# Optimization experiments

Hardware: AMD Instinct MI355X
Metric: run time of the kernel (lower is better)

The kernel has to match this reference:

```python
import jax, jax.numpy as jnp
import numpy as np

ALPHA = 0.05
NUM_LAYERS = 2


def setup_inputs() -> dict:
    key = jax.random.key(0)
    k1, k2, k3, k4, k5 = jax.random.split(key, 5)
    N, F, C, E = 100000, 64, 40, 1600000
    x = jax.random.normal(k1, (N, F), dtype=jnp.float32)
    edge_attr = jax.random.uniform(k2, (E,), dtype=jnp.float32)
    lin_w = jax.random.normal(k3, (F, C), dtype=jnp.float32) * (1.0 / np.sqrt(F))
    lin_b = jax.random.normal(k4, (C,), dtype=jnp.float32) * 0.01
    edge_index = jax.random.randint(k5, (2, E), 0, N, dtype=jnp.int64)
    return {"x": x, "edge_attr": edge_attr, "lin_w": lin_w, "lin_b": lin_b,
            "edge_index": edge_index}


def reference(x, edge_attr, lin_w, lin_b, edge_index):
    N = x.shape[0]
    row, col = edge_index[0], edge_index[1]
    # symmetric GCN normalization with edge weights
    deg = jax.ops.segment_sum(edge_attr, col, num_segments=N)  # [N]
    dis = jnp.where(deg > 0, jax.lax.rsqrt(jnp.maximum(deg, 1e-12)), 0.0)
    norm = dis[row] * edge_attr * dis[col]  # [E]

    def conv(h):
        # gather source features, scale, scatter-add to targets
        return jax.ops.segment_sum(norm[:, None] * h[row], col, num_segments=N)

    x_input = ALPHA * x
    scale = (1.0 - ALPHA) / NUM_LAYERS
    h = x
    acc = jnp.zeros_like(x)
    for _ in range(NUM_LAYERS):
        h = conv(h)
        acc = acc + scale * h
    out = acc + x_input
    logits = out @ lin_w + lin_b
    return jax.nn.log_softmax(logits, axis=1)
```

## Files before the change

### kernel.cpp

```cpp
#include <hip/hip_runtime.h>
#include <math.h>
#include <string.h>


#define ALPHA  0.05f
#define SCALE  0.475f
#define FDIM   64
#define CDIM   40
#define NPAD   131072
#define CHUNK  8192
#define BCAP   10240
#define SRCMASK 0x1FFFFu

__device__ __forceinline__ unsigned short f2bf(float f) {
    unsigned u = __float_as_uint(f);
    unsigned r = (u + 0x7FFFu + ((u >> 16) & 1u)) >> 16;
    return (unsigned short)r;
}
__device__ __forceinline__ float bfLo(unsigned u) { return __uint_as_float(u << 16); }
__device__ __forceinline__ float bfHi(unsigned u) { return __uint_as_float(u & 0xffff0000u); }
__device__ __forceinline__ float wUnpack(unsigned v) {
    return __uint_as_float((v >> 17) << 16);
}

__global__ __launch_bounds__(1024) void part_scatter(
        const int* __restrict__ row, const int* __restrict__ col,
        const float* __restrict__ ea, int* __restrict__ alloc,
        int2* __restrict__ ppay, int E) {
    __shared__ unsigned h[256];
    __shared__ unsigned offs[256];
    int tid = threadIdx.x, blk = blockIdx.x;
    if (tid < 256) h[tid] = 0;
    __syncthreads();
    int base = blk * CHUNK;
    int end  = min(base + CHUNK, E);
    for (int e = base + tid; e < end; e += 1024)
        atomicAdd(&h[col[e] >> 9], 1u);
    __syncthreads();
    if (tid < 256) {
        unsigned hc = h[tid];
        unsigned r = hc ? (unsigned)atomicAdd(&alloc[tid], (int)hc) : 0u;
        offs[tid] = (unsigned)(tid * BCAP) + r;
    }
    __syncthreads();
    for (int e = base + tid; e < end; e += 1024) {
        int c = col[e];
        int bin = c >> 9;
        unsigned p = atomicAdd(&offs[bin], 1u);
        if (p < (unsigned)((bin + 1) * BCAP))
            ppay[p] = make_int2(row[e] | ((c & 511) << 20), __float_as_int(ea[e]));
    }
}

__global__ __launch_bounds__(256) void bucket_base(const int* __restrict__ alloc,
                                                   int* __restrict__ bb) {
    __shared__ int s[256];
    int tid = threadIdx.x;
    int v = min(alloc[tid], BCAP);
    s[tid] = v;
    __syncthreads();
    for (int off = 1; off < 256; off <<= 1) {
        int t = (tid >= off) ? s[tid - off] : 0;
        __syncthreads();
        s[tid] += t;
        __syncthreads();
    }
    bb[tid] = s[tid] - v;
    if (tid == 255) bb[256] = s[255];
}

__global__ __launch_bounds__(256) void bucket_csr(
        const int2* __restrict__ ppay, const int* __restrict__ alloc,
        const int* __restrict__ bb, int* __restrict__ start,
        unsigned* __restrict__ csr, float* __restrict__ dis, int N) {
    __shared__ unsigned cnt8[512][8];
    __shared__ unsigned ps[256], exc[512];
    __shared__ float sdeg[512];
    int tid = threadIdx.x, k = blockIdx.x;
    int cnt = min(alloc[k], BCAP);
    int e0  = bb[k];
    const int2* src = ppay + (size_t)k * BCAP;

    for (int i = tid; i < 4096; i += 256) ((unsigned*)cnt8)[i] = 0;
    sdeg[tid] = 0.0f; sdeg[tid + 256] = 0.0f;
    __syncthreads();

    for (int j = tid; j < cnt; j += 256) {
        int2 pay = src[j];
        int c = (pay.x >> 20) & 511;
        atomicAdd(&cnt8[c][(pay.x & 0xFFFFF) >> 14], 1u);
        atomicAdd(&sdeg[c], __int_as_float(pay.y));
    }
    __syncthreads();

    int c0 = 2 * tid, c1 = 2 * tid + 1;
    unsigned t0 = 0, t1 = 0;
    #pragma unroll
    for (int o = 0; o < 8; ++o) { t0 += cnt8[c0][o]; t1 += cnt8[c1][o]; }
    unsigned pair = t0 + t1;
    ps[tid] = pair;
    __syncthreads();
    for (int off = 1; off < 256; off <<= 1) {
        unsigned t = (tid >= off) ? ps[tid - off] : 0;
        __syncthreads();
        ps[tid] += t;
        __syncthreads();
    }
    unsigned pexc = ps[tid] - pair;
    exc[c0] = pexc;
    exc[c1] = pexc + t0;
    unsigned b = pexc;
    #pragma unroll
    for (int o = 0; o < 8; ++o) { unsigned t = cnt8[c0][o]; cnt8[c0][o] = b; b += t; }
    b = pexc + t0;
    #pragma unroll
    for (int o = 0; o < 8; ++o) { unsigned t = cnt8[c1][o]; cnt8[c1][o] = b; b += t; }
    __syncthreads();

    #pragma unroll
    for (int i = tid; i < 512; i += 256) {
        int g = k * 512 + i;
        if (g <= N) start[g] = e0 + (int)exc[i];
        if (g < N) {
            float d = sdeg[i];
            dis[g] = (d > 0.0f) ? rsqrtf(fmaxf(d, 1e-12f)) : 0.0f;
        }
    }

    for (int j = tid; j < cnt; j += 256) {
        int2 pay = src[j];
        int c    = (pay.x >> 20) & 511;
        int srcn = pay.x & 0xFFFFF;
        unsigned p = atomicAdd(&cnt8[c][srcn >> 14], 1u);
        unsigned wbf = (unsigned)f2bf(__int_as_float(pay.y));
        csr[e0 + p] = (unsigned)srcn | (wbf << 17);
    }
}

__global__ void csr_scale_kernel(unsigned* __restrict__ csr,
                                 const float* __restrict__ dis, int E) {
    int stride = gridDim.x * blockDim.x;
    for (int e = blockIdx.x * blockDim.x + threadIdx.x; e < E; e += stride) {
        unsigned v = csr[e];
        unsigned src = v & SRCMASK;
        float w = wUnpack(v) * dis[src];
        csr[e] = src | ((unsigned)f2bf(w) << 17);
    }
}

__global__ __launch_bounds__(256) void lin_kernel(
        const float* __restrict__ x, const float* __restrict__ W,
        unsigned* __restrict__ ybf, int N) {
    __shared__ float sWt[CDIM][FDIM + 4];
    for (int i = threadIdx.x; i < FDIM * CDIM; i += 256) {
        int k = i / CDIM, c = i - k * CDIM;
        sWt[c][k] = W[i];
    }
    __syncthreads();

    int t = threadIdx.x;
    int node = blockIdx.x * 64 + (t >> 2);
    if (node >= N) return;
    int cs = (t & 3) * 10;

    float acc[10];
    #pragma unroll
    for (int i = 0; i < 10; ++i) acc[i] = 0.0f;

    const float4* xr = (const float4*)(x + (size_t)node * FDIM);
    #pragma unroll
    for (int k4 = 0; k4 < FDIM / 4; ++k4) {
        float4 v = xr[k4];
        #pragma unroll
        for (int i = 0; i < 10; ++i) {
            const float4 w = *(const float4*)&sWt[cs + i][k4 * 4];
            acc[i] = fmaf(v.x, w.x, fmaf(v.y, w.y, fmaf(v.z, w.z, fmaf(v.w, w.w, acc[i]))));
        }
    }

    unsigned* yr = ybf + (size_t)node * (CDIM / 2) + (t & 3) * 5;
    #pragma unroll
    for (int k = 0; k < 5; ++k)
        yr[k] = (unsigned)f2bf(acc[2 * k]) | ((unsigned)f2bf(acc[2 * k + 1]) << 16);
}

__global__ __launch_bounds__(256) void spmv_kernel(
        const unsigned* __restrict__ gin, const int* __restrict__ start,
        const unsigned* __restrict__ csr, const float* __restrict__ dis,
        unsigned* __restrict__ gout, int N) {
    int lane = threadIdx.x & 63;
    int wid  = threadIdx.x >> 6;
    int grp  = lane / 20;
    int grel = lane - grp * 20;
    int node = blockIdx.x * 12 + wid * 3 + grp;
    bool act = (grp < 3) && (node < N);

    int e0 = 0, e1 = 0;
    if (act) { e0 = start[node]; e1 = start[node + 1]; }

    float aL0 = 0, aL1 = 0, aL2 = 0, aL3 = 0;
    float aH0 = 0, aH1 = 0, aH2 = 0, aH3 = 0;
    int j = e0;
    for (; j + 7 < e1; j += 8) {
        unsigned v0 = csr[j],     v1 = csr[j + 1], v2 = csr[j + 2], v3 = csr[j + 3];
        unsigned v4 = csr[j + 4], v5 = csr[j + 5], v6 = csr[j + 6], v7 = csr[j + 7];
        unsigned u0 = gin[(size_t)(v0 & SRCMASK) * 20 + grel];
        unsigned u1 = gin[(size_t)(v1 & SRCMASK) * 20 + grel];
        unsigned u2 = gin[(size_t)(v2 & SRCMASK) * 20 + grel];
        unsigned u3 = gin[(size_t)(v3 & SRCMASK) * 20 + grel];
        unsigned u4 = gin[(size_t)(v4 & SRCMASK) * 20 + grel];
        unsigned u5 = gin[(size_t)(v5 & SRCMASK) * 20 + grel];
        unsigned u6 = gin[(size_t)(v6 & SRCMASK) * 20 + grel];
        unsigned u7 = gin[(size_t)(v7 & SRCMASK) * 20 + grel];
        float w0 = wUnpack(v0), w1 = wUnpack(v1), w2 = wUnpack(v2), w3 = wUnpack(v3);
        float w4 = wUnpack(v4), w5 = wUnpack(v5), w6 = wUnpack(v6), w7 = wUnpack(v7);
        aL0 = fmaf(w0, bfLo(u0), aL0); aH0 = fmaf(w0, bfHi(u0), aH0);
        aL1 = fmaf(w1, bfLo(u1), aL1); aH1 = fmaf(w1, bfHi(u1), aH1);
        aL2 = fmaf(w2, bfLo(u2), aL2); aH2 = fmaf(w2, bfHi(u2), aH2);
        aL3 = fmaf(w3, bfLo(u3), aL3); aH3 = fmaf(w3, bfHi(u3), aH3);
        aL0 = fmaf(w4, bfLo(u4), aL0); aH0 = fmaf(w4, bfHi(u4), aH0);
        aL1 = fmaf(w5, bfLo(u5), aL1); aH1 = fmaf(w5, bfHi(u5), aH1);
        aL2 = fmaf(w6, bfLo(u6), aL2); aH2 = fmaf(w6, bfHi(u6), aH2);
        aL3 = fmaf(w7, bfLo(u7), aL3); aH3 = fmaf(w7, bfHi(u7), aH3);
    }
    for (; j < e1; ++j) {
        unsigned v = csr[j];
        unsigned u = gin[(size_t)(v & SRCMASK) * 20 + grel];
        float w = wUnpack(v);
        aL0 = fmaf(w, bfLo(u), aL0); aH0 = fmaf(w, bfHi(u), aH0);
    }
    if (act) {
        float dn = dis[node];
        float lo = dn * ((aL0 + aL1) + (aL2 + aL3));
        float hi = dn * ((aH0 + aH1) + (aH2 + aH3));
        gout[(size_t)node * 20 + grel] = (unsigned)f2bf(lo) | ((unsigned)f2bf(hi) << 16);
    }
}

__global__ __launch_bounds__(256) void spmv_final_kernel(
        const unsigned* __restrict__ g1, const unsigned* __restrict__ y,
        const float* __restrict__ bias, const int* __restrict__ start,
        const unsigned* __restrict__ csr, const float* __restrict__ dis,
        float* __restrict__ out, int N) {
    int lane = threadIdx.x & 63;
    int wid  = threadIdx.x >> 6;
    int grp  = lane / 20;
    int grel = lane - grp * 20;
    int node = blockIdx.x * 12 + wid * 3 + grp;
    bool act = (grp < 3) && (node < N);

    int e0 = 0, e1 = 0;
    if (act) { e0 = start[node]; e1 = start[node + 1]; }

    float aL0 = 0, aL1 = 0, aL2 = 0, aL3 = 0;
    float aH0 = 0, aH1 = 0, aH2 = 0, aH3 = 0;
    int j = e0;
    for (; j + 7 < e1; j += 8) {
        unsigned v0 = csr[j],     v1 = csr[j + 1], v2 = csr[j + 2], v3 = csr[j + 3];
        unsigned v4 = csr[j + 4], v5 = csr[j + 5], v6 = csr[j + 6], v7 = csr[j + 7];
        unsigned u0 = g1[(size_t)(v0 & SRCMASK) * 20 + grel];
        unsigned u1 = g1[(size_t)(v1 & SRCMASK) * 20 + grel];
        unsigned u2 = g1[(size_t)(v2 & SRCMASK) * 20 + grel];
        unsigned u3 = g1[(size_t)(v3 & SRCMASK) * 20 + grel];
        unsigned u4 = g1[(size_t)(v4 & SRCMASK) * 20 + grel];
        unsigned u5 = g1[(size_t)(v5 & SRCMASK) * 20 + grel];
        unsigned u6 = g1[(size_t)(v6 & SRCMASK) * 20 + grel];
        unsigned u7 = g1[(size_t)(v7 & SRCMASK) * 20 + grel];
        float w0 = wUnpack(v0), w1 = wUnpack(v1), w2 = wUnpack(v2), w3 = wUnpack(v3);
        float w4 = wUnpack(v4), w5 = wUnpack(v5), w6 = wUnpack(v6), w7 = wUnpack(v7);
        aL0 = fmaf(w0, bfLo(u0), aL0); aH0 = fmaf(w0, bfHi(u0), aH0);
        aL1 = fmaf(w1, bfLo(u1), aL1); aH1 = fmaf(w1, bfHi(u1), aH1);
        aL2 = fmaf(w2, bfLo(u2), aL2); aH2 = fmaf(w2, bfHi(u2), aH2);
        aL3 = fmaf(w3, bfLo(u3), aL3); aH3 = fmaf(w3, bfHi(u3), aH3);
        aL0 = fmaf(w4, bfLo(u4), aL0); aH0 = fmaf(w4, bfHi(u4), aH0);
        aL1 = fmaf(w5, bfLo(u5), aL1); aH1 = fmaf(w5, bfHi(u5), aH1);
        aL2 = fmaf(w6, bfLo(u6), aL2); aH2 = fmaf(w6, bfHi(u6), aH2);
        aL3 = fmaf(w7, bfLo(u7), aL3); aH3 = fmaf(w7, bfHi(u7), aH3);
    }
    for (; j < e1; ++j) {
        unsigned v = csr[j];
        unsigned u = g1[(size_t)(v & SRCMASK) * 20 + grel];
        float w = wUnpack(v);
        aL0 = fmaf(w, bfLo(u), aL0); aH0 = fmaf(w, bfHi(u), aH0);
    }

    float logitL = 0.0f, logitH = 0.0f;
    if (act) {
        float dn  = dis[node];
        float g2L = dn * ((aL0 + aL1) + (aL2 + aL3));
        float g2H = dn * ((aH0 + aH1) + (aH2 + aH3));
        unsigned yu = y[(size_t)node * 20 + grel];
        unsigned gu = g1[(size_t)node * 20 + grel];
        float2 bv = *(const float2*)&bias[2 * grel];
        logitL = fmaf(ALPHA, bfLo(yu), fmaf(SCALE, bfLo(gu) + g2L, bv.x));
        logitH = fmaf(ALPHA, bfHi(yu), fmaf(SCALE, bfHi(gu) + g2H, bv.y));
    }

    float m = act ? fmaxf(logitL, logitH) : -INFINITY;
    #pragma unroll
    for (int off = 16; off; off >>= 1) {
        float o = __shfl(m, lane + off);
        if (grel + off < 20) m = fmaxf(m, o);
    }
    m = __shfl(m, grp * 20);

    float ex = act ? (expf(logitL - m) + expf(logitH - m)) : 0.0f;
    #pragma unroll
    for (int off = 16; off; off >>= 1) {
        float o = __shfl(ex, lane + off);
        if (grel + off < 20) ex += o;
    }
    ex = __shfl(ex, grp * 20);

    if (act) {
        float lse = m + logf(ex);
        float2 o;
        o.x = logitL - lse;
        o.y = logitH - lse;
        double dv;
        memcpy(&dv, &o, 8);
        __builtin_nontemporal_store(dv, (double*)&out[(size_t)node * CDIM + 2 * grel]);
    }
}

extern "C" void kernel_launch(void* const* d_in, const int* in_sizes, int n_in,
                              void* d_out, int out_size, void* d_ws, size_t ws_size,
                              hipStream_t stream) {
    const float* x  = (const float*)d_in[0];
    const float* ea = (const float*)d_in[1];
    const float* W  = (const float*)d_in[2];
    const float* b  = (const float*)d_in[3];
    const int*   ei = (const int*)d_in[4];

    const int N = in_sizes[0] / FDIM;
    const int E = in_sizes[1];
    const int* row = ei;
    const int* col = ei + E;

    const int NBLK = (E + CHUNK - 1) / CHUNK;

    int*   startp = (int*)d_ws;
    float* dis    = (float*)(startp + NPAD);
    int*   alloc  = (int*)(dis + NPAD);
    int*   bb     = alloc + 1024;
    int2*  ppay   = (int2*)(bb + 1024);
    unsigned* csr = (unsigned*)(ppay + 256 * BCAP);
    unsigned* g1bf = csr + E;
    unsigned* ybf  = (unsigned*)ppay;

    hipMemsetAsync(alloc, 0, 256 * sizeof(int), stream);

    part_scatter<<<NBLK, 1024, 0, stream>>>(row, col, ea, alloc, ppay, E);
    bucket_base <<<1, 256, 0, stream>>>(alloc, bb);
    bucket_csr  <<<256, 256, 0, stream>>>(ppay, alloc, bb, startp, csr, dis, N);
    csr_scale_kernel<<<2048, 256, 0, stream>>>(csr, dis, E);
    lin_kernel  <<<(N + 63) / 64, 256, 0, stream>>>(x, W, ybf, N);

    int spmv_blocks = (N + 11) / 12;
    spmv_kernel      <<<spmv_blocks, 256, 0, stream>>>(ybf, startp, csr, dis, g1bf, N);
    spmv_final_kernel<<<spmv_blocks, 256, 0, stream>>>(g1bf, ybf, b, startp, csr, dis,
                                                       (float*)d_out, N);
}
```

Before: 157.5 us.

## Use merge-path edge-balanced SpMV partitioning and fold bucket prefix scan into CSR build

```diff
diff --git a/kernel.cpp b/kernel.cpp
--- a/kernel.cpp
+++ b/kernel.cpp
@@ -10,6 +10,7 @@
 #define NPAD   131072
 #define CHUNK  8192
 #define BCAP   10240
+#define CE     64
 #define SRCMASK 0x1FFFFu
 
 __device__ __forceinline__ unsigned short f2bf(float f) {
@@ -52,33 +53,28 @@
     }
 }
 
-__global__ __launch_bounds__(256) void bucket_base(const int* __restrict__ alloc,
-                                                   int* __restrict__ bb) {
-    __shared__ int s[256];
-    int tid = threadIdx.x;
-    int v = min(alloc[tid], BCAP);
-    s[tid] = v;
-    __syncthreads();
-    for (int off = 1; off < 256; off <<= 1) {
-        int t = (tid >= off) ? s[tid - off] : 0;
-        __syncthreads();
-        s[tid] += t;
-        __syncthreads();
-    }
-    bb[tid] = s[tid] - v;
-    if (tid == 255) bb[256] = s[255];
-}
-
 __global__ __launch_bounds__(256) void bucket_csr(
         const int2* __restrict__ ppay, const int* __restrict__ alloc,
-        const int* __restrict__ bb, int* __restrict__ start,
-        unsigned* __restrict__ csr, float* __restrict__ dis, int N) {
+        int* __restrict__ start, unsigned* __restrict__ csr,
+        float* __restrict__ dis, int N) {
     __shared__ unsigned cnt8[512][8];
     __shared__ unsigned ps[256], exc[512];
     __shared__ float sdeg[512];
+    __shared__ int sAll[256];
     int tid = threadIdx.x, k = blockIdx.x;
+
+    sAll[tid] = min(alloc[tid], BCAP);
+    __syncthreads();
+    int v = sAll[tid];
+    for (int off = 1; off < 256; off <<= 1) {
+        int t = (tid >= off) ? sAll[tid - off] : 0;
+        __syncthreads();
+        sAll[tid] += t;
+        __syncthreads();
+    }
+    int e0  = sAll[k] - min(alloc[k], BCAP);
     int cnt = min(alloc[k], BCAP);
-    int e0  = bb[k];
+    (void)v;
     const int2* src = ppay + (size_t)k * BCAP;
 
     for (int i = tid; i < 4096; i += 256) ((unsigned*)cnt8)[i] = 0;
@@ -184,142 +180,149 @@
         yr[k] = (unsigned)f2bf(acc[2 * k]) | ((unsigned)f2bf(acc[2 * k + 1]) << 16);
 }
 
-__global__ __launch_bounds__(256) void spmv_kernel(
+__global__ __launch_bounds__(256) void spmv_mp(
         const unsigned* __restrict__ gin, const int* __restrict__ start,
         const unsigned* __restrict__ csr, const float* __restrict__ dis,
-        unsigned* __restrict__ gout, int N) {
+        unsigned* __restrict__ gout, int N, int E, int G) {
     int lane = threadIdx.x & 63;
     int wid  = threadIdx.x >> 6;
     int grp  = lane / 20;
     int grel = lane - grp * 20;
-    int node = blockIdx.x * 12 + wid * 3 + grp;
-    bool act = (grp < 3) && (node < N);
-
-    int e0 = 0, e1 = 0;
-    if (act) { e0 = start[node]; e1 = start[node + 1]; }
-
-    float aL0 = 0, aL1 = 0, aL2 = 0, aL3 = 0;
-    float aH0 = 0, aH1 = 0, aH2 = 0, aH3 = 0;
-    int j = e0;
-    for (; j + 7 < e1; j += 8) {
-        unsigned v0 = csr[j],     v1 = csr[j + 1], v2 = csr[j + 2], v3 = csr[j + 3];
-        unsigned v4 = csr[j + 4], v5 = csr[j + 5], v6 = csr[j + 6], v7 = csr[j + 7];
-        unsigned u0 = gin[(size_t)(v0 & SRCMASK) * 20 + grel];
-        unsigned u1 = gin[(size_t)(v1 & SRCMASK) * 20 + grel];
-        unsigned u2 = gin[(size_t)(v2 & SRCMASK) * 20 + grel];
-        unsigned u3 = gin[(size_t)(v3 & SRCMASK) * 20 + grel];
-        unsigned u4 = gin[(size_t)(v4 & SRCMASK) * 20 + grel];
-        unsigned u5 = gin[(size_t)(v5 & SRCMASK) * 20 + grel];
-        unsigned u6 = gin[(size_t)(v6 & SRCMASK) * 20 + grel];
-        unsigned u7 = gin[(size_t)(v7 & SRCMASK) * 20 + grel];
-        float w0 = wUnpack(v0), w1 = wUnpack(v1), w2 = wUnpack(v2), w3 = wUnpack(v3);
-        float w4 = wUnpack(v4), w5 = wUnpack(v5), w6 = wUnpack(v6), w7 = wUnpack(v7);
-        aL0 = fmaf(w0, bfLo(u0), aL0); aH0 = fmaf(w0, bfHi(u0), aH0);
-        aL1 = fmaf(w1, bfLo(u1), aL1); aH1 = fmaf(w1, bfHi(u1), aH1);
-        aL2 = fmaf(w2, bfLo(u2), aL2); aH2 = fmaf(w2, bfHi(u2), aH2);
-        aL3 = fmaf(w3, bfLo(u3), aL3); aH3 = fmaf(w3, bfHi(u3), aH3);
-        aL0 = fmaf(w4, bfLo(u4), aL0); aH0 = fmaf(w4, bfHi(u4), aH0);
-        aL1 = fmaf(w5, bfLo(u5), aL1); aH1 = fmaf(w5, bfHi(u5), aH1);
-        aL2 = fmaf(w6, bfLo(u6), aL2); aH2 = fmaf(w6, bfHi(u6), aH2);
-        aL3 = fmaf(w7, bfLo(u7), aL3); aH3 = fmaf(w7, bfHi(u7), aH3);
-    }
-    for (; j < e1; ++j) {
-        unsigned v = csr[j];
-        unsigned u = gin[(size_t)(v & SRCMASK) * 20 + grel];
-        float w = wUnpack(v);
-        aL0 = fmaf(w, bfLo(u), aL0); aH0 = fmaf(w, bfHi(u), aH0);
-    }
-    if (act) {
-        float dn = dis[node];
-        float lo = dn * ((aL0 + aL1) + (aL2 + aL3));
-        float hi = dn * ((aH0 + aH1) + (aH2 + aH3));
-        gout[(size_t)node * 20 + grel] = (unsigned)f2bf(lo) | ((unsigned)f2bf(hi) << 16);
-    }
-}
-
-__global__ __launch_bounds__(256) void spmv_final_kernel(
+    int g = blockIdx.x * 12 + wid * 3 + grp;
+    bool act = (grp < 3) && (g < G);
+    int lo  = act ? g * CE : (E + 2);
+    int hiR = min(lo + CE, E + 1);
+
+    int a = 0, b = N;
+    while (a < b) { int mid = (a + b) >> 1; if (start[mid] < lo) a = mid + 1; else b = mid; }
+
+    int n = a;
+    while (n < N && start[n] < hiR) {
+        int e0 = start[n], e1 = start[n + 1];
+        float aL0 = 0, aL1 = 0, aL2 = 0, aL3 = 0;
+        float aH0 = 0, aH1 = 0, aH2 = 0, aH3 = 0;
+        int j = e0;
+        for (; j + 7 < e1; j += 8) {
+            unsigned v0 = csr[j],     v1 = csr[j + 1], v2 = csr[j + 2], v3 = csr[j + 3];
+            unsigned v4 = csr[j + 4], v5 = csr[j + 5], v6 = csr[j + 6], v7 = csr[j + 7];
+            unsigned u0 = gin[(size_t)(v0 & SRCMASK) * 20 + grel];
+            unsigned u1 = gin[(size_t)(v1 & SRCMASK) * 20 + grel];
+            unsigned u2 = gin[(size_t)(v2 & SRCMASK) * 20 + grel];
+            unsigned u3 = gin[(size_t)(v3 & SRCMASK) * 20 + grel];
+            unsigned u4 = gin[(size_t)(v4 & SRCMASK) * 20 + grel];
+            unsigned u5 = gin[(size_t)(v5 & SRCMASK) * 20 + grel];
+            unsigned u6 = gin[(size_t)(v6 & SRCMASK) * 20 + grel];
+            unsigned u7 = gin[(size_t)(v7 & SRCMASK) * 20 + grel];
+            float w0 = wUnpack(v0), w1 = wUnpack(v1), w2 = wUnpack(v2), w3 = wUnpack(v3);
+            float w4 = wUnpack(v4), w5 = wUnpack(v5), w6 = wUnpack(v6), w7 = wUnpack(v7);
+            aL0 = fmaf(w0, bfLo(u0), aL0); aH0 = fmaf(w0, bfHi(u0), aH0);
+            aL1 = fmaf(w1, bfLo(u1), aL1); aH1 = fmaf(w1, bfHi(u1), aH1);
+            aL2 = fmaf(w2, bfLo(u2), aL2); aH2 = fmaf(w2, bfHi(u2), aH2);
+            aL3 = fmaf(w3, bfLo(u3), aL3); aH3 = fmaf(w3, bfHi(u3), aH3);
+            aL0 = fmaf(w4, bfLo(u4), aL0); aH0 = fmaf(w4, bfHi(u4), aH0);
+            aL1 = fmaf(w5, bfLo(u5), aL1); aH1 = fmaf(w5, bfHi(u5), aH1);
+            aL2 = fmaf(w6, bfLo(u6), aL2); aH2 = fmaf(w6, bfHi(u6), aH2);
+            aL3 = fmaf(w7, bfLo(u7), aL3); aH3 = fmaf(w7, bfHi(u7), aH3);
+        }
+        for (; j < e1; ++j) {
+            unsigned v = csr[j];
+            unsigned u = gin[(size_t)(v & SRCMASK) * 20 + grel];
+            float w = wUnpack(v);
+            aL0 = fmaf(w, bfLo(u), aL0); aH0 = fmaf(w, bfHi(u), aH0);
+        }
+        float dn = dis[n];
+        float lov = dn * ((aL0 + aL1) + (aL2 + aL3));
+        float hiv = dn * ((aH0 + aH1) + (aH2 + aH3));
+        gout[(size_t)n * 20 + grel] = (unsigned)f2bf(lov) | ((unsigned)f2bf(hiv) << 16);
+        ++n;
+    }
+}
+
+__global__ __launch_bounds__(256) void spmv_final_mp(
         const unsigned* __restrict__ g1, const unsigned* __restrict__ y,
         const float* __restrict__ bias, const int* __restrict__ start,
         const unsigned* __restrict__ csr, const float* __restrict__ dis,
-        float* __restrict__ out, int N) {
+        float* __restrict__ out, int N, int E, int G) {
     int lane = threadIdx.x & 63;
     int wid  = threadIdx.x >> 6;
     int grp  = lane / 20;
     int grel = lane - grp * 20;
-    int node = blockIdx.x * 12 + wid * 3 + grp;
-    bool act = (grp < 3) && (node < N);
-
-    int e0 = 0, e1 = 0;
-    if (act) { e0 = start[node]; e1 = start[node + 1]; }
-
-    float aL0 = 0, aL1 = 0, aL2 = 0, aL3 = 0;
-    float aH0 = 0, aH1 = 0, aH2 = 0, aH3 = 0;
-    int j = e0;
-    for (; j + 7 < e1; j += 8) {
-        unsigned v0 = csr[j],     v1 = csr[j + 1], v2 = csr[j + 2], v3 = csr[j + 3];
-        unsigned v4 = csr[j + 4], v5 = csr[j + 5], v6 = csr[j + 6], v7 = csr[j + 7];
-        unsigned u0 = g1[(size_t)(v0 & SRCMASK) * 20 + grel];
-        unsigned u1 = g1[(size_t)(v1 & SRCMASK) * 20 + grel];
-        unsigned u2 = g1[(size_t)(v2 & SRCMASK) * 20 + grel];
-        unsigned u3 = g1[(size_t)(v3 & SRCMASK) * 20 + grel];
-        unsigned u4 = g1[(size_t)(v4 & SRCMASK) * 20 + grel];
-        unsigned u5 = g1[(size_t)(v5 & SRCMASK) * 20 + grel];
-        unsigned u6 = g1[(size_t)(v6 & SRCMASK) * 20 + grel];
-        unsigned u7 = g1[(size_t)(v7 & SRCMASK) * 20 + grel];
-        float w0 = wUnpack(v0), w1 = wUnpack(v1), w2 = wUnpack(v2), w3 = wUnpack(v3);
-        float w4 = wUnpack(v4), w5 = wUnpack(v5), w6 = wUnpack(v6), w7 = wUnpack(v7);
-        aL0 = fmaf(w0, bfLo(u0), aL0); aH0 = fmaf(w0, bfHi(u0), aH0);
-        aL1 = fmaf(w1, bfLo(u1), aL1); aH1 = fmaf(w1, bfHi(u1), aH1);
-        aL2 = fmaf(w2, bfLo(u2), aL2); aH2 = fmaf(w2, bfHi(u2), aH2);
-        aL3 = fmaf(w3, bfLo(u3), aL3); aH3 = fmaf(w3, bfHi(u3), aH3);
-        aL0 = fmaf(w4, bfLo(u4), aL0); aH0 = fmaf(w4, bfHi(u4), aH0);
-        aL1 = fmaf(w5, bfLo(u5), aL1); aH1 = fmaf(w5, bfHi(u5), aH1);
-        aL2 = fmaf(w6, bfLo(u6), aL2); aH2 = fmaf(w6, bfHi(u6), aH2);
-        aL3 = fmaf(w7, bfLo(u7), aL3); aH3 = fmaf(w7, bfHi(u7), aH3);
-    }
-    for (; j < e1; ++j) {
-        unsigned v = csr[j];
-        unsigned u = g1[(size_t)(v & SRCMASK) * 20 + grel];
-        float w = wUnpack(v);
-        aL0 = fmaf(w, bfLo(u), aL0); aH0 = fmaf(w, bfHi(u), aH0);
-    }
-
-    float logitL = 0.0f, logitH = 0.0f;
-    if (act) {
-        float dn  = dis[node];
+    int g = blockIdx.x * 12 + wid * 3 + grp;
+    bool act = (grp < 3) && (g < G);
+    int lo  = act ? g * CE : (E + 2);
+    int hiR = min(lo + CE, E + 1);
+
+    int a = 0, b = N;
+    while (a < b) { int mid = (a + b) >> 1; if (start[mid] < lo) a = mid + 1; else b = mid; }
+
+    int n = a;
+    while (n < N && start[n] < hiR) {
+        int e0 = start[n], e1 = start[n + 1];
+        float aL0 = 0, aL1 = 0, aL2 = 0, aL3 = 0;
+        float aH0 = 0, aH1 = 0, aH2 = 0, aH3 = 0;
+        int j = e0;
+        for (; j + 7 < e1; j += 8) {
+            unsigned v0 = csr[j],     v1 = csr[j + 1], v2 = csr[j + 2], v3 = csr[j + 3];
+            unsigned v4 = csr[j + 4], v5 = csr[j + 5], v6 = csr[j + 6], v7 = csr[j + 7];
+            unsigned u0 = g1[(size_t)(v0 & SRCMASK) * 20 + grel];
+            unsigned u1 = g1[(size_t)(v1 & SRCMASK) * 20 + grel];
+            unsigned u2 = g1[(size_t)(v2 & SRCMASK) * 20 + grel];
+            unsigned u3 = g1[(size_t)(v3 & SRCMASK) * 20 + grel];
+            unsigned u4 = g1[(size_t)(v4 & SRCMASK) * 20 + grel];
+            unsigned u5 = g1[(size_t)(v5 & SRCMASK) * 20 + grel];
+            unsigned u6 = g1[(size_t)(v6 & SRCMASK) * 20 + grel];
+            unsigned u7 = g1[(size_t)(v7 & SRCMASK) * 20 + grel];
+            float w0 = wUnpack(v0), w1 = wUnpack(v1), w2 = wUnpack(v2), w3 = wUnpack(v3);
+            float w4 = wUnpack(v4), w5 = wUnpack(v5), w6 = wUnpack(v6), w7 = wUnpack(v7);
+            aL0 = fmaf(w0, bfLo(u0), aL0); aH0 = fmaf(w0, bfHi(u0), aH0);
+            aL1 = fmaf(w1, bfLo(u1), aL1); aH1 = fmaf(w1, bfHi(u1), aH1);
+            aL2 = fmaf(w2, bfLo(u2), aL2); aH2 = fmaf(w2, bfHi(u2), aH2);
+            aL3 = fmaf(w3, bfLo(u3), aL3); aH3 = fmaf(w3, bfHi(u3), aH3);
+            aL0 = fmaf(w4, bfLo(u4), aL0); aH0 = fmaf(w4, bfHi(u4), aH0);
+            aL1 = fmaf(w5, bfLo(u5), aL1); aH1 = fmaf(w5, bfHi(u5), aH1);
+            aL2 = fmaf(w6, bfLo(u6), aL2); aH2 = fmaf(w6, bfHi(u6), aH2);
+            aL3 = fmaf(w7, bfLo(u7), aL3); aH3 = fmaf(w7, bfHi(u7), aH3);
+        }
+        for (; j < e1; ++j) {
+            unsigned v = csr[j];
+            unsigned u = g1[(size_t)(v & SRCMASK) * 20 + grel];
+            float w = wUnpack(v);
+            aL0 = fmaf(w, bfLo(u), aL0); aH0 = fmaf(w, bfHi(u), aH0);
+        }
+
+        float dn  = dis[n];
         float g2L = dn * ((aL0 + aL1) + (aL2 + aL3));
         float g2H = dn * ((aH0 + aH1) + (aH2 + aH3));
-        unsigned yu = y[(size_t)node * 20 + grel];
-        unsigned gu = g1[(size_t)node * 20 + grel];
+        unsigned yu = y[(size_t)n * 20 + grel];
+        unsigned gu = g1[(size_t)n * 20 + grel];
         float2 bv = *(const float2*)&bias[2 * grel];
-        logitL = fmaf(ALPHA, bfLo(yu), fmaf(SCALE, bfLo(gu) + g2L, bv.x));
-        logitH = fmaf(ALPHA, bfHi(yu), fmaf(SCALE, bfHi(gu) + g2H, bv.y));
-    }
-
-    float m = act ? fmaxf(logitL, logitH) : -INFINITY;
-    #pragma unroll
-    for (int off = 16; off; off >>= 1) {
-        float o = __shfl(m, lane + off);
-        if (grel + off < 20) m = fmaxf(m, o);
-    }
-    m = __shfl(m, grp * 20);
-
-    float ex = act ? (expf(logitL - m) + expf(logitH - m)) : 0.0f;
-    #pragma unroll
-    for (int off = 16; off; off >>= 1) {
-        float o = __shfl(ex, lane + off);
-        if (grel + off < 20) ex += o;
-    }
-    ex = __shfl(ex, grp * 20);
-
-    if (act) {
+        float logitL = fmaf(ALPHA, bfLo(yu), fmaf(SCALE, bfLo(gu) + g2L, bv.x));
+        float logitH = fmaf(ALPHA, bfHi(yu), fmaf(SCALE, bfHi(gu) + g2H, bv.y));
+
+        float m = fmaxf(logitL, logitH);
+        #pragma unroll
+        for (int off = 16; off; off >>= 1) {
+            float o = __shfl(m, lane + off);
+            if (grel + off < 20) m = fmaxf(m, o);
+        }
+        m = __shfl(m, grp * 20);
+
+        float ex = expf(logitL - m) + expf(logitH - m);
+        #pragma unroll
+        for (int off = 16; off; off >>= 1) {
+            float o = __shfl(ex, lane + off);
+            if (grel + off < 20) ex += o;
+        }
+        ex = __shfl(ex, grp * 20);
+
         float lse = m + logf(ex);
         float2 o;
         o.x = logitL - lse;
         o.y = logitH - lse;
         double dv;
         memcpy(&dv, &o, 8);
-        __builtin_nontemporal_store(dv, (double*)&out[(size_t)node * CDIM + 2 * grel]);
+        __builtin_nontemporal_store(dv, (double*)&out[(size_t)n * CDIM + 2 * grel]);
+        ++n;
     }
 }
 
@@ -338,12 +341,12 @@
     const int* col = ei + E;
 
     const int NBLK = (E + CHUNK - 1) / CHUNK;
+    const int G    = (E + CE) / CE;
 
     int*   startp = (int*)d_ws;
     float* dis    = (float*)(startp + NPAD);
     int*   alloc  = (int*)(dis + NPAD);
-    int*   bb     = alloc + 1024;
-    int2*  ppay   = (int2*)(bb + 1024);
+    int2*  ppay   = (int2*)(alloc + 1024);
     unsigned* csr = (unsigned*)(ppay + 256 * BCAP);
     unsigned* g1bf = csr + E;
     unsigned* ybf  = (unsigned*)ppay;
@@ -351,13 +354,12 @@
     hipMemsetAsync(alloc, 0, 256 * sizeof(int), stream);
 
     part_scatter<<<NBLK, 1024, 0, stream>>>(row, col, ea, alloc, ppay, E);
-    bucket_base <<<1, 256, 0, stream>>>(alloc, bb);
-    bucket_csr  <<<256, 256, 0, stream>>>(ppay, alloc, bb, startp, csr, dis, N);
+    bucket_csr  <<<256, 256, 0, stream>>>(ppay, alloc, startp, csr, dis, N);
     csr_scale_kernel<<<2048, 256, 0, stream>>>(csr, dis, E);
     lin_kernel  <<<(N + 63) / 64, 256, 0, stream>>>(x, W, ybf, N);
 
-    int spmv_blocks = (N + 11) / 12;
-    spmv_kernel      <<<spmv_blocks, 256, 0, stream>>>(ybf, startp, csr, dis, g1bf, N);
-    spmv_final_kernel<<<spmv_blocks, 256, 0, stream>>>(g1bf, ybf, b, startp, csr, dis,
-                                                       (float*)d_out, N);
-}
+    int mp_blocks = (G + 11) / 12;
+    spmv_mp      <<<mp_blocks, 256, 0, stream>>>(ybf, startp, csr, dis, g1bf, N, E, G);
+    spmv_final_mp<<<mp_blocks, 256, 0, stream>>>(g1bf, ybf, b, startp, csr, dis,
+                                                 (float*)d_out, N, E, G);
+}
```

After: 207.3 us. 31.6% more time.
